# Optimization experiments

Measured on AMD Instinct MI355X. Metric: run time of the kernel, lower is better.

Reference implementation:

```python
import jax, jax.numpy as jnp
import numpy as np

N_NODES = 50000
N_EDGES = 500000
D_IN, D_HID = 128, 256


def _add_self_loops(edge_index, n):
    loop = jnp.arange(n, dtype=edge_index.dtype)
    src = jnp.concatenate([edge_index[0], loop])
    dst = jnp.concatenate([edge_index[1], loop])
    return src, dst


def _gcn_layer(x, W, b, src, dst, dinv_sqrt, n):
    # x: [N, d_in] -> h: [N, d_out]
    h = x @ W
    # symmetric normalization D^{-1/2} (A+I) D^{-1/2}
    norm = dinv_sqrt[src] * dinv_sqrt[dst]          # [E+N]
    msg = h[src] * norm[:, None]                    # gather + scale
    agg = jax.ops.segment_sum(msg, dst, num_segments=n)  # scatter-add
    return agg + b


def setup_inputs() -> dict:
    key = jax.random.key(0)
    ks = jax.random.split(key, 8)
    x = jax.random.normal(ks[0], (N_NODES, D_IN), dtype=jnp.float32)
    edge_index = jax.random.randint(ks[1], (2, N_EDGES), 0, N_NODES, dtype=jnp.int64 if jax.config.read('jax_enable_x64') else jnp.int32)
    s = lambda fan_in: 1.0 / np.sqrt(fan_in)
    W1 = jax.random.uniform(ks[2], (D_IN, D_HID), jnp.float32, -s(D_IN), s(D_IN))
    b1 = jnp.zeros((D_HID,), jnp.float32)
    W2 = jax.random.uniform(ks[3], (D_HID, D_HID), jnp.float32, -s(D_HID), s(D_HID))
    b2 = jnp.zeros((D_HID,), jnp.float32)
    W3 = jax.random.uniform(ks[4], (D_HID, D_HID), jnp.float32, -s(D_HID), s(D_HID))
    b3 = jnp.zeros((D_HID,), jnp.float32)
    return {"x": x, "edge_index": edge_index, "W1": W1, "b1": b1,
            "W2": W2, "b2": b2, "W3": W3, "b3": b3}


def reference(x, edge_index, W1, b1, W2, b2, W3, b3):
    n = x.shape[0]
    src, dst = _add_self_loops(edge_index, n)
    # degree includes self loops (edge weight 1), as in torch_geometric GCNConv
    deg = jax.ops.segment_sum(jnp.ones_like(dst, dtype=x.dtype), dst, num_segments=n)
    dinv_sqrt = jnp.where(deg > 0, jax.lax.rsqrt(jnp.maximum(deg, 1e-12)), 0.0)
    h = jax.nn.relu(_gcn_layer(x, W1, b1, src, dst, dinv_sqrt, n))
    h = jax.nn.relu(_gcn_layer(h, W2, b2, src, dst, dinv_sqrt, n))
    h = _gcn_layer(h, W3, b3, src, dst, dinv_sqrt, n)
    return h
```

## Files before the change

kernel.cpp:

```cpp
#include <hip/hip_runtime.h>

#define NNODES 50000
#define NEDGES 500000
#define DIN 128
#define DHID 256
#define MPAD 50048
#define NI4 12500
#define NSB 49

typedef unsigned short u16;
typedef __attribute__((ext_vector_type(8))) _Float16 half8;
typedef __attribute__((ext_vector_type(4))) float f32x4;

__device__ __forceinline__ u16 f2h(float f) {
  union { _Float16 h; u16 u; } v; v.h = (_Float16)f; return v.u;
}
__device__ __forceinline__ float h2f(unsigned int u) {
  union { _Float16 h; u16 u; } v; v.u = (u16)u; return (float)v.h;
}

#define GLDS16(g, l) __builtin_amdgcn_global_load_lds( \
    (const __attribute__((address_space(1))) void*)(g), \
    (__attribute__((address_space(3))) void*)(l), 16, 0, 0)

__global__ void k_zero_i32(int* __restrict__ p, int n) {
  int i = blockIdx.x * blockDim.x + threadIdx.x;
  if (i < n) p[i] = 0;
}

__global__ void k_hist(const int* __restrict__ dst, int* __restrict__ deg, int e) {
  int i = blockIdx.x * blockDim.x + threadIdx.x;
  if (i < e) atomicAdd(&deg[dst[i]], 1);
}

__global__ __launch_bounds__(256) void k_blocksum(const int* __restrict__ deg,
                                                  int* __restrict__ partials) {
  __shared__ int red[256];
  int tid = threadIdx.x;
  int t4 = blockIdx.x * 256 + tid;
  int sum = 0;
  if (t4 < NI4) {
    int4 v = ((const int4*)deg)[t4];
    sum = v.x + v.y + v.z + v.w;
  }
  red[tid] = sum;
  __syncthreads();
  for (int off = 128; off > 0; off >>= 1) {
    if (tid < off) red[tid] += red[tid + off];
    __syncthreads();
  }
  if (tid == 0) partials[blockIdx.x] = red[0];
}

__global__ __launch_bounds__(256) void k_scan2(int* __restrict__ deg,
                                               const int* __restrict__ partials,
                                               int* __restrict__ row_ptr,
                                               float* __restrict__ dinv) {
  __shared__ int sdata[256];
  __shared__ int sprefix;
  int tid = threadIdx.x, bid = blockIdx.x;
  int t4 = bid * 256 + tid;
  int4 v = make_int4(0, 0, 0, 0);
  if (t4 < NI4) v = ((const int4*)deg)[t4];
  int tsum = v.x + v.y + v.z + v.w;
  sdata[tid] = tsum;
  if (tid == 0) {
    int pre = 0;
    for (int b = 0; b < bid; ++b) pre += partials[b];
    sprefix = pre;
  }
  __syncthreads();
  for (int off = 1; off < 256; off <<= 1) {
    int val = (tid >= off) ? sdata[tid - off] : 0;
    __syncthreads();
    sdata[tid] += val;
    __syncthreads();
  }
  if (t4 < NI4) {
    int run = sdata[tid] - tsum + sprefix;
    int base = t4 * 4;
    float4 dv;
    dv.x = rsqrtf((float)v.x + 1.0f);
    dv.y = rsqrtf((float)v.y + 1.0f);
    dv.z = rsqrtf((float)v.z + 1.0f);
    dv.w = rsqrtf((float)v.w + 1.0f);
    *(float4*)(dinv + base) = dv;
    row_ptr[base + 0] = run; run += v.x;
    row_ptr[base + 1] = run; run += v.y;
    row_ptr[base + 2] = run; run += v.z;
    row_ptr[base + 3] = run; run += v.w;
    if (base + 4 == NNODES) row_ptr[NNODES] = run;
    ((int4*)deg)[t4] = make_int4(0, 0, 0, 0);
  }
}

__global__ void k_fill(const int* __restrict__ src, const int* __restrict__ dst,
                       const float* __restrict__ dinv, const int* __restrict__ row_ptr,
                       int* __restrict__ cursor, int* __restrict__ csr_src,
                       float* __restrict__ csr_nrm, int e) {
  int i = blockIdx.x * blockDim.x + threadIdx.x;
  if (i < e) {
    int d = dst[i], s = src[i];
    int pos = row_ptr[d] + atomicAdd(&cursor[d], 1);
    csr_src[pos] = s;
    csr_nrm[pos] = dinv[s] * dinv[d];
  }
}

__global__ void k_x2f16(const float* __restrict__ x, u16* __restrict__ xh, int total4) {
  int i = blockIdx.x * blockDim.x + threadIdx.x;
  if (i >= total4) return;
  float4 v = ((const float4*)x)[i];
  ushort4 o;
  o.x = f2h(v.x); o.y = f2h(v.y); o.z = f2h(v.z); o.w = f2h(v.w);
  ((ushort4*)xh)[i] = o;
}

__global__ void k_splitW3(const float* __restrict__ W1f, u16* __restrict__ P1,
                          const float* __restrict__ W2f, u16* __restrict__ P2,
                          const float* __restrict__ W3f, u16* __restrict__ P3) {
  int i = blockIdx.x * blockDim.x + threadIdx.x;
  const int s1 = DIN * 256, s2 = s1 + DHID * 256, s3 = s2 + DHID * 256;
  if (i >= s3) return;
  const float* W; u16* P; int li;
  if (i < s1)      { W = W1f; P = P1; li = i; }
  else if (i < s2) { W = W2f; P = P2; li = i - s1; }
  else             { W = W3f; P = P3; li = i - s2; }
  int k = li >> 8, n = li & 255;
  int t = k >> 5, q = (k >> 3) & 3, j = k & 7;
  int c = n >> 4, m = n & 15;
  int f = (c * 64 + q * 16 + m) * 8 + j;
  float w = W[li] * 256.0f;
  u16 hi = f2h(w);
  u16 lo = f2h(w - h2f(hi));
  P[(size_t)t * 16384 + f] = hi;
  P[(size_t)t * 16384 + 8192 + f] = lo;
}

template<int W>
__global__ __launch_bounds__(256) void k_aggG(const u16* __restrict__ hf,
                                              const float* __restrict__ dinv,
                                              const int* __restrict__ row_ptr,
                                              const int* __restrict__ csr_src,
                                              const float* __restrict__ csr_nrm,
                                              u16* __restrict__ aout, int n) {
  constexpr int GL = W / 8;
  constexpr int NG = 64 / GL;
  const int lane = threadIdx.x & 63;
  const int wave = threadIdx.x >> 6;
  const int g = lane / GL;
  const int sub = lane % GL;
  const int coff = sub * 8;

  for (int node = blockIdx.x * 4 + wave; node < n; node += gridDim.x * 4) {
    float acc[8];
    float di = dinv[node];
    float s2 = (g == 0) ? di * di : 0.0f;

    auto ldrow = [&](int row, float* v) {
      const uint4 u = *(const uint4*)(hf + (size_t)row * W + coff);
      v[0] = h2f(u.x & 0xffffu); v[1] = h2f(u.x >> 16);
      v[2] = h2f(u.y & 0xffffu); v[3] = h2f(u.y >> 16);
      v[4] = h2f(u.z & 0xffffu); v[5] = h2f(u.z >> 16);
      v[6] = h2f(u.w & 0xffffu); v[7] = h2f(u.w >> 16);
    };

    {
      float v[8];
      ldrow(node, v);
#pragma unroll
      for (int j = 0; j < 8; ++j) acc[j] = s2 * v[j];
    }

    const int p1 = row_ptr[node + 1];
    int e = row_ptr[node] + g;
    for (; e + NG < p1; e += 2 * NG) {
      int s0 = csr_src[e], s1 = csr_src[e + NG];
      float w0 = csr_nrm[e], w1 = csr_nrm[e + NG];
      float v0[8], v1[8];
      ldrow(s0, v0); ldrow(s1, v1);
#pragma unroll
      for (int j = 0; j < 8; ++j) {
        acc[j] = fmaf(w0, v0[j], acc[j]);
        acc[j] = fmaf(w1, v1[j], acc[j]);
      }
    }
    if (e < p1) {
      int s = csr_src[e];
      float w = csr_nrm[e];
      float v[8];
      ldrow(s, v);
#pragma unroll
      for (int j = 0; j < 8; ++j) acc[j] = fmaf(w, v[j], acc[j]);
    }

#pragma unroll
    for (int j = 0; j < 8; ++j) {
      if constexpr (NG == 4) acc[j] += __shfl_xor(acc[j], 16);
      acc[j] += __shfl_xor(acc[j], 32);
    }

    if (g == 0) {
      uint4 o;
      o.x = (unsigned)f2h(acc[0]) | ((unsigned)f2h(acc[1]) << 16);
      o.y = (unsigned)f2h(acc[2]) | ((unsigned)f2h(acc[3]) << 16);
      o.z = (unsigned)f2h(acc[4]) | ((unsigned)f2h(acc[5]) << 16);
      o.w = (unsigned)f2h(acc[6]) | ((unsigned)f2h(acc[7]) << 16);
      *(uint4*)(aout + (size_t)node * W + coff) = o;
    }
  }
}

template<int K, int EPI>
__global__ __launch_bounds__(256, 4) void k_gemm_mfma(const u16* __restrict__ A,
                                                      const u16* __restrict__ Bpk,
                                                      const float* __restrict__ bias,
                                                      u16* __restrict__ hf16,
                                                      float* __restrict__ outf) {
  __shared__ __align__(16) u16 Bs[16384];
  const int lane = threadIdx.x & 63;
  const int wave = threadIdx.x >> 6;
  const int rw = wave & 1, cw = wave >> 1;
  const int m0 = blockIdx.x * 64 + rw * 32;

  f32x4 acc0[8], acc1[8];
#pragma unroll
  for (int c = 0; c < 8; ++c) {
    acc0[c] = {0.f, 0.f, 0.f, 0.f};
    acc1[c] = {0.f, 0.f, 0.f, 0.f};
  }

  const u16* a0p = A + (size_t)(m0 + (lane & 15)) * K + ((lane >> 4) * 8);
  const u16* a1p = a0p + (size_t)16 * K;

  for (int t = 0; t < K / 32; ++t) {
    __syncthreads();
    {
      const char* gsrc = (const char*)(Bpk + (size_t)t * 16384);
      char* lbase = (char*)Bs;
#pragma unroll
      for (int it = 0; it < 8; ++it) {
        int off = (wave * 8 + it) * 1024 + lane * 16;
        GLDS16(gsrc + off, lbase + off);
      }
    }
    __syncthreads();

    half8 a0 = *(const half8*)(a0p + t * 32);
    half8 a1 = *(const half8*)(a1p + t * 32);
#pragma unroll
    for (int c = 0; c < 8; ++c) {
      const u16* fb = Bs + ((cw * 8 + c) * 64 + lane) * 8;
      half8 bh = *(const half8*)fb;
      half8 bl = *(const half8*)(fb + 8192);
      acc0[c] = __builtin_amdgcn_mfma_f32_16x16x32_f16(a0, bh, acc0[c], 0, 0, 0);
      acc0[c] = __builtin_amdgcn_mfma_f32_16x16x32_f16(a0, bl, acc0[c], 0, 0, 0);
      acc1[c] = __builtin_amdgcn_mfma_f32_16x16x32_f16(a1, bh, acc1[c], 0, 0, 0);
      acc1[c] = __builtin_amdgcn_mfma_f32_16x16x32_f16(a1, bl, acc1[c], 0, 0, 0);
    }
  }

  const int cbase = lane & 15;
  const int r0 = m0 + ((lane >> 4) * 4);
  const float sc = 1.0f / 256.0f;
#pragma unroll
  for (int c = 0; c < 8; ++c) {
    int col = (cw * 8 + c) * 16 + cbase;
    float bv = bias[col];
#pragma unroll
    for (int r = 0; r < 4; ++r) {
      float v0 = fmaf(acc0[c][r], sc, bv);
      float v1 = fmaf(acc1[c][r], sc, bv);
      if (EPI == 0) {
        v0 = fmaxf(v0, 0.f);
        v1 = fmaxf(v1, 0.f);
        hf16[(size_t)(r0 + r) * 256 + col] = f2h(v0);
        hf16[(size_t)(r0 + 16 + r) * 256 + col] = f2h(v1);
      } else {
        if (r0 + r < NNODES) outf[(size_t)(r0 + r) * 256 + col] = v0;
        if (r0 + 16 + r < NNODES) outf[(size_t)(r0 + 16 + r) * 256 + col] = v1;
      }
    }
  }
}

extern "C" void kernel_launch(void* const* d_in, const int* in_sizes, int n_in,
                              void* d_out, int out_size, void* d_ws, size_t ws_size,
                              hipStream_t stream) {
  const float* x  = (const float*)d_in[0];
  const int*   ei = (const int*)d_in[1];
  const float* W1 = (const float*)d_in[2];
  const float* b1 = (const float*)d_in[3];
  const float* W2 = (const float*)d_in[4];
  const float* b2 = (const float*)d_in[5];
  const float* W3 = (const float*)d_in[6];
  const float* b3 = (const float*)d_in[7];
  float* out = (float*)d_out;
  (void)in_sizes; (void)n_in; (void)out_size; (void)ws_size;

  char* ws = (char*)d_ws;
  size_t off = 0;
  auto alloc = [&](size_t bytes) -> void* {
    void* p = (void*)(ws + off);
    off += (bytes + 255) & ~(size_t)255;
    return p;
  };
  float* dinv    = (float*)alloc((size_t)NNODES * 4);
  int*   deg     = (int*)alloc((size_t)NNODES * 4);
  int*   row_ptr = (int*)alloc((size_t)(NNODES + 1) * 4);
  int*   partials= (int*)alloc((size_t)NSB * 4);
  int*   csr_src = (int*)alloc((size_t)NEDGES * 4);
  float* csr_nrm = (float*)alloc((size_t)NEDGES * 4);
  u16*   xh      = (u16*)alloc((size_t)NNODES * DIN * 2);
  u16*   hbuf    = (u16*)alloc((size_t)MPAD * 256 * 2);
  u16*   A1      = (u16*)alloc((size_t)MPAD * DIN * 2);
  u16*   A2      = (u16*)alloc((size_t)MPAD * 256 * 2);
  u16*   W1pk    = (u16*)alloc((size_t)(DIN / 32) * 16384 * 2);
  u16*   W2pk    = (u16*)alloc((size_t)(DHID / 32) * 16384 * 2);
  u16*   W3pk    = (u16*)alloc((size_t)(DHID / 32) * 16384 * 2);

  const int* e_src = ei;
  const int* e_dst = ei + NEDGES;

  const int tb = 256;
  k_zero_i32<<<(NNODES + tb - 1) / tb, tb, 0, stream>>>(deg, NNODES);
  k_hist<<<(NEDGES + tb - 1) / tb, tb, 0, stream>>>(e_dst, deg, NEDGES);
  k_blocksum<<<NSB, 256, 0, stream>>>(deg, partials);
  k_scan2<<<NSB, 256, 0, stream>>>(deg, partials, row_ptr, dinv);
  k_fill<<<(NEDGES + tb - 1) / tb, tb, 0, stream>>>(e_src, e_dst, dinv, row_ptr, deg,
                                                    csr_src, csr_nrm, NEDGES);

  int x4 = NNODES * DIN / 4;
  k_x2f16<<<(x4 + tb - 1) / tb, tb, 0, stream>>>(x, xh, x4);
  int wtot = (DIN + DHID + DHID) * 256;
  k_splitW3<<<(wtot + tb - 1) / tb, tb, 0, stream>>>(W1, W1pk, W2, W2pk, W3, W3pk);

  const int gblocks = MPAD / 64;
  const int aggrid = 2048;

  k_aggG<128><<<aggrid, 256, 0, stream>>>(xh, dinv, row_ptr, csr_src, csr_nrm,
                                          A1, NNODES);
  k_gemm_mfma<DIN, 0><<<gblocks, 256, 0, stream>>>(A1, W1pk, b1, hbuf, nullptr);
  k_aggG<256><<<aggrid, 256, 0, stream>>>(hbuf, dinv, row_ptr, csr_src, csr_nrm,
                                          A2, NNODES);
  k_gemm_mfma<DHID, 0><<<gblocks, 256, 0, stream>>>(A2, W2pk, b2, hbuf, nullptr);
  k_aggG<256><<<aggrid, 256, 0, stream>>>(hbuf, dinv, row_ptr, csr_src, csr_nrm,
                                          A2, NNODES);
  k_gemm_mfma<DHID, 1><<<gblocks, 256, 0, stream>>>(A2, W3pk, b3, nullptr, out);
}
```

Before: 339.1 us.

## Assign one node per lane group in aggregation and unroll edge loop by four

```diff
diff --git a/kernel.cpp b/kernel.cpp
--- a/kernel.cpp
+++ b/kernel.cpp
@@ -138,7 +138,7 @@
 }
 
 template<int W>
-__global__ __launch_bounds__(256) void k_aggG(const u16* __restrict__ hf,
+__global__ __launch_bounds__(256) void k_aggN(const u16* __restrict__ hf,
                                               const float* __restrict__ dinv,
                                               const int* __restrict__ row_ptr,
                                               const int* __restrict__ csr_src,
@@ -152,62 +152,50 @@
   const int sub = lane % GL;
   const int coff = sub * 8;
 
-  for (int node = blockIdx.x * 4 + wave; node < n; node += gridDim.x * 4) {
+  const int base = (blockIdx.x * 4 + wave) * NG + g;
+  const int stride = gridDim.x * 4 * NG;
+
+  for (int node = base; node < n; node += stride) {
     float acc[8];
     float di = dinv[node];
-    float s2 = (g == 0) ? di * di : 0.0f;
-
-    auto ldrow = [&](int row, float* v) {
-      const uint4 u = *(const uint4*)(hf + (size_t)row * W + coff);
-      v[0] = h2f(u.x & 0xffffu); v[1] = h2f(u.x >> 16);
-      v[2] = h2f(u.y & 0xffffu); v[3] = h2f(u.y >> 16);
-      v[4] = h2f(u.z & 0xffffu); v[5] = h2f(u.z >> 16);
-      v[6] = h2f(u.w & 0xffffu); v[7] = h2f(u.w >> 16);
-    };
+    float s2 = di * di;
 
     {
-      float v[8];
-      ldrow(node, v);
-#pragma unroll
-      for (int j = 0; j < 8; ++j) acc[j] = s2 * v[j];
-    }
-
+      half8 v = *(const half8*)(hf + (size_t)node * W + coff);
+#pragma unroll
+      for (int j = 0; j < 8; ++j) acc[j] = s2 * (float)v[j];
+    }
+
+    const int p0 = row_ptr[node];
     const int p1 = row_ptr[node + 1];
-    int e = row_ptr[node] + g;
-    for (; e + NG < p1; e += 2 * NG) {
-      int s0 = csr_src[e], s1 = csr_src[e + NG];
-      float w0 = csr_nrm[e], w1 = csr_nrm[e + NG];
-      float v0[8], v1[8];
-      ldrow(s0, v0); ldrow(s1, v1);
+    for (int e = p0; e < p1; e += 4) {
+      int i1 = e + 1 < p1 ? e + 1 : e;
+      int i2 = e + 2 < p1 ? e + 2 : e;
+      int i3 = e + 3 < p1 ? e + 3 : e;
+      int s0i = csr_src[e], s1i = csr_src[i1], s2i = csr_src[i2], s3i = csr_src[i3];
+      float w0 = csr_nrm[e];
+      float w1 = e + 1 < p1 ? csr_nrm[i1] : 0.0f;
+      float w2 = e + 2 < p1 ? csr_nrm[i2] : 0.0f;
+      float w3 = e + 3 < p1 ? csr_nrm[i3] : 0.0f;
+      half8 v0 = *(const half8*)(hf + (size_t)s0i * W + coff);
+      half8 v1 = *(const half8*)(hf + (size_t)s1i * W + coff);
+      half8 v2 = *(const half8*)(hf + (size_t)s2i * W + coff);
+      half8 v3 = *(const half8*)(hf + (size_t)s3i * W + coff);
 #pragma unroll
       for (int j = 0; j < 8; ++j) {
-        acc[j] = fmaf(w0, v0[j], acc[j]);
-        acc[j] = fmaf(w1, v1[j], acc[j]);
+        acc[j] = fmaf(w0, (float)v0[j], acc[j]);
+        acc[j] = fmaf(w1, (float)v1[j], acc[j]);
+        acc[j] = fmaf(w2, (float)v2[j], acc[j]);
+        acc[j] = fmaf(w3, (float)v3[j], acc[j]);
       }
     }
-    if (e < p1) {
-      int s = csr_src[e];
-      float w = csr_nrm[e];
-      float v[8];
-      ldrow(s, v);
-#pragma unroll
-      for (int j = 0; j < 8; ++j) acc[j] = fmaf(w, v[j], acc[j]);
-    }
-
-#pragma unroll
-    for (int j = 0; j < 8; ++j) {
-      if constexpr (NG == 4) acc[j] += __shfl_xor(acc[j], 16);
-      acc[j] += __shfl_xor(acc[j], 32);
-    }
-
-    if (g == 0) {
-      uint4 o;
-      o.x = (unsigned)f2h(acc[0]) | ((unsigned)f2h(acc[1]) << 16);
-      o.y = (unsigned)f2h(acc[2]) | ((unsigned)f2h(acc[3]) << 16);
-      o.z = (unsigned)f2h(acc[4]) | ((unsigned)f2h(acc[5]) << 16);
-      o.w = (unsigned)f2h(acc[6]) | ((unsigned)f2h(acc[7]) << 16);
-      *(uint4*)(aout + (size_t)node * W + coff) = o;
-    }
+
+    uint4 o;
+    o.x = (unsigned)f2h(acc[0]) | ((unsigned)f2h(acc[1]) << 16);
+    o.y = (unsigned)f2h(acc[2]) | ((unsigned)f2h(acc[3]) << 16);
+    o.z = (unsigned)f2h(acc[4]) | ((unsigned)f2h(acc[5]) << 16);
+    o.w = (unsigned)f2h(acc[6]) | ((unsigned)f2h(acc[7]) << 16);
+    *(uint4*)(aout + (size_t)node * W + coff) = o;
   }
 }
 
@@ -338,13 +326,13 @@
   const int gblocks = MPAD / 64;
   const int aggrid = 2048;
 
-  k_aggG<128><<<aggrid, 256, 0, stream>>>(xh, dinv, row_ptr, csr_src, csr_nrm,
+  k_aggN<128><<<aggrid, 256, 0, stream>>>(xh, dinv, row_ptr, csr_src, csr_nrm,
                                           A1, NNODES);
   k_gemm_mfma<DIN, 0><<<gblocks, 256, 0, stream>>>(A1, W1pk, b1, hbuf, nullptr);
-  k_aggG<256><<<aggrid, 256, 0, stream>>>(hbuf, dinv, row_ptr, csr_src, csr_nrm,
+  k_aggN<256><<<aggrid, 256, 0, stream>>>(hbuf, dinv, row_ptr, csr_src, csr_nrm,
                                           A2, NNODES);
   k_gemm_mfma<DHID, 0><<<gblocks, 256, 0, stream>>>(A2, W2pk, b2, hbuf, nullptr);
-  k_aggG<256><<<aggrid, 256, 0, stream>>>(hbuf, dinv, row_ptr, csr_src, csr_nrm,
+  k_aggN<256><<<aggrid, 256, 0, stream>>>(hbuf, dinv, row_ptr, csr_src, csr_nrm,
                                           A2, NNODES);
   k_gemm_mfma<DHID, 1><<<gblocks, 256, 0, stream>>>(A2, W3pk, b3, nullptr, out);
 }
```

After: 337.3 us. No clear change (-0.5%).
